# Kernel optimization log

Hardware: AMD Instinct MI355X
Metric: run time of the kernel (lower is better)

## Reference

```python
import jax, jax.numpy as jnp
import numpy as np

B, S, D_IN, D_OUT = 2, 2048, 4096, 4096


def setup_inputs() -> dict:
    key = jax.random.key(0)
    kx, kw, kb = jax.random.split(key, 3)
    x = jax.random.normal(kx, (B, S, D_IN), dtype=jnp.float32)
    weight = jax.random.normal(kw, (D_OUT, D_IN), dtype=jnp.float32)
    bias = jax.random.normal(kb, (D_OUT,), dtype=jnp.float32)
    return {"x": x, "weight": weight, "bias": bias}


def reference(x, weight, bias):
    # FdaBinary forward is simply sign(); linear with binarized weight.
    w_bin = jnp.sign(weight)  # [D_OUT, D_IN], values in {-1, 0, +1}
    # F.linear: x @ w.T + b
    out = jnp.einsum("bsd,od->bso", x, w_bin) + bias
    return out
```

## Files before the change

### kernel.cpp

```cpp
#include <hip/hip_runtime.h>
#include <hip/hip_bf16.h>
#include <stdint.h>
#include <stddef.h>

#define M_DIM 4096
#define N_DIM 4096
#define K_DIM 4096
#define BM 128
#define BN 128
#define BK 64
#define NKT (K_DIM / BK)

typedef __bf16 bf16;
typedef __attribute__((ext_vector_type(4))) __bf16 bf16x4;
typedef __attribute__((ext_vector_type(8))) __bf16 bf16x8;
typedef __attribute__((ext_vector_type(4))) float f32x4;

__global__ __launch_bounds__(256) void prep_kernel(const float* __restrict__ x,
                                                   const float* __restrict__ w,
                                                   bf16* __restrict__ xb,
                                                   bf16* __restrict__ wb) {
    const int idx = blockIdx.x * 256 + threadIdx.x;
    float4 xv = ((const float4*)x)[idx];
    bf16x4 xo;
    xo[0] = (bf16)xv.x; xo[1] = (bf16)xv.y; xo[2] = (bf16)xv.z; xo[3] = (bf16)xv.w;
    ((bf16x4*)xb)[idx] = xo;

    float4 wv = ((const float4*)w)[idx];
    bf16x4 wo;
    wo[0] = (bf16)((wv.x > 0.f) ? 1.f : ((wv.x < 0.f) ? -1.f : 0.f));
    wo[1] = (bf16)((wv.y > 0.f) ? 1.f : ((wv.y < 0.f) ? -1.f : 0.f));
    wo[2] = (bf16)((wv.z > 0.f) ? 1.f : ((wv.z < 0.f) ? -1.f : 0.f));
    wo[3] = (bf16)((wv.w > 0.f) ? 1.f : ((wv.w < 0.f) ? -1.f : 0.f));
    ((bf16x4*)wb)[idx] = wo;
}

__device__ __forceinline__ void load_lds16(const void* g, void* l) {
    __builtin_amdgcn_global_load_lds(
        (const __attribute__((address_space(1))) void*)g,
        (__attribute__((address_space(3))) void*)l, 16, 0, 0);
}

__global__ __launch_bounds__(256) void gemm_bin_kernel(const bf16* __restrict__ A,
                                                       const bf16* __restrict__ Bw,
                                                       const float* __restrict__ bias,
                                                       float* __restrict__ C) {
    __shared__ __align__(16) bf16 As[BM * BK];
    __shared__ __align__(16) bf16 Bs[BN * BK];

    const int tid  = threadIdx.x;
    const int lane = tid & 63;
    const int wave = tid >> 6;
    const int wm   = wave & 1;
    const int wn   = wave >> 1;

    const int tileM = blockIdx.y * BM;
    const int tileN = blockIdx.x * BN;

    const int rowInC = lane >> 3;
    const int q_src  = (lane & 7) ^ rowInC;

    const bf16* gA[4];
    const bf16* gB[4];
    bf16* lA[4];
    bf16* lB[4];
#pragma unroll
    for (int t = 0; t < 4; ++t) {
        const int c = wave * 4 + t;
        gA[t] = A  + (size_t)(tileM + c * 8 + rowInC) * K_DIM + q_src * 8;
        gB[t] = Bw + (size_t)(tileN + c * 8 + rowInC) * K_DIM + q_src * 8;
        lA[t] = As + c * 512;
        lB[t] = Bs + c * 512;
    }

    f32x4 acc[4][4];
#pragma unroll
    for (int i = 0; i < 4; ++i)
#pragma unroll
        for (int j = 0; j < 4; ++j)
            acc[i][j] = (f32x4){0.f, 0.f, 0.f, 0.f};

    const int l15 = lane & 15;
    const int qf  = lane >> 4;
    const int fragRowA = wm * 64 + l15;
    const int fragRowB = wn * 64 + l15;

    for (int kt = 0; kt < NKT; ++kt) {
#pragma unroll
        for (int t = 0; t < 4; ++t) {
            load_lds16(gA[t], lA[t]);
            load_lds16(gB[t], lB[t]);
            gA[t] += BK; gB[t] += BK;
        }

        __syncthreads();

#pragma unroll
        for (int kk = 0; kk < 2; ++kk) {
            const int s = (kk * 4 + qf) ^ (l15 & 7);
            bf16x8 af[4], bfr[4];
#pragma unroll
            for (int i = 0; i < 4; ++i)
                af[i] = *(const bf16x8*)&As[(fragRowA + i * 16) * BK + s * 8];
#pragma unroll
            for (int j = 0; j < 4; ++j)
                bfr[j] = *(const bf16x8*)&Bs[(fragRowB + j * 16) * BK + s * 8];

#pragma unroll
            for (int i = 0; i < 4; ++i)
#pragma unroll
                for (int j = 0; j < 4; ++j)
                    acc[i][j] = __builtin_amdgcn_mfma_f32_16x16x32_bf16(af[i], bfr[j], acc[i][j], 0, 0, 0);
        }

        __syncthreads();
    }

#pragma unroll
    for (int j = 0; j < 4; ++j) {
        const int col = tileN + wn * 64 + j * 16 + l15;
        const float bv = bias[col];
#pragma unroll
        for (int i = 0; i < 4; ++i) {
            const int row0 = tileM + wm * 64 + i * 16 + (qf << 2);
#pragma unroll
            for (int rr = 0; rr < 4; ++rr) {
                C[(size_t)(row0 + rr) * N_DIM + col] = acc[i][j][rr] + bv;
            }
        }
    }
}

extern "C" void kernel_launch(void* const* d_in, const int* in_sizes, int n_in,
                              void* d_out, int out_size, void* d_ws, size_t ws_size,
                              hipStream_t stream) {
    const float* x    = (const float*)d_in[0];
    const float* w    = (const float*)d_in[1];
    const float* bias = (const float*)d_in[2];
    float* out        = (float*)d_out;

    const int nElem = M_DIM * K_DIM;
    bf16* xb = (bf16*)d_ws;
    bf16* wb = xb + (size_t)nElem;

    prep_kernel<<<nElem / 4 / 256, 256, 0, stream>>>(x, w, xb, wb);

    dim3 grid(N_DIM / BN, M_DIM / BM);
    gemm_bin_kernel<<<grid, 256, 0, stream>>>(xb, wb, bias, out);
}
```

Before: 296.4 us.

## Enlarge GEMM tile to 256x256 with 8 waves and double-buffered LDS pipeline

Raises the block tile to 256x256 with 512 threads and double-buffers the LDS tiles. Each K-tile is split into four phases that interleave direct-to-LDS loads for the next tile with MFMA work, using explicit vmcnt waits, s_barrier and setprio. This is meant to hide global-load latency and raise arithmetic intensity per block. The cost is more registers per thread (32 accumulators), fewer blocks in the grid (256 tiles), and fragile hand-written wait counts.

```diff
diff --git a/kernel.cpp b/kernel.cpp
--- a/kernel.cpp
+++ b/kernel.cpp
@@ -6,10 +6,12 @@
 #define M_DIM 4096
 #define N_DIM 4096
 #define K_DIM 4096
-#define BM 128
-#define BN 128
+#define BM 256
+#define BN 256
 #define BK 64
 #define NKT (K_DIM / BK)
+#define BKB (BK * 2)
+#define RSTRIDE ((size_t)64 * K_DIM * 2)
 
 typedef __bf16 bf16;
 typedef __attribute__((ext_vector_type(4))) __bf16 bf16x4;
@@ -41,79 +43,108 @@
         (__attribute__((address_space(3))) void*)l, 16, 0, 0);
 }
 
-__global__ __launch_bounds__(256) void gemm_bin_kernel(const bf16* __restrict__ A,
-                                                       const bf16* __restrict__ Bw,
-                                                       const float* __restrict__ bias,
-                                                       float* __restrict__ C) {
-    __shared__ __align__(16) bf16 As[BM * BK];
-    __shared__ __align__(16) bf16 Bs[BN * BK];
+__global__ __launch_bounds__(512, 2) void gemm_bin_kernel(const bf16* __restrict__ A,
+                                                          const bf16* __restrict__ Bw,
+                                                          const float* __restrict__ bias,
+                                                          float* __restrict__ C) {
+    __shared__ __align__(16) bf16 As[2][BM * BK];
+    __shared__ __align__(16) bf16 Bs[2][BM * BK];
 
     const int tid  = threadIdx.x;
     const int lane = tid & 63;
     const int wave = tid >> 6;
-    const int wm   = wave & 1;
-    const int wn   = wave >> 1;
+    const int wm   = wave >> 2;
+    const int wn   = wave & 3;
 
     const int tileM = blockIdx.y * BM;
     const int tileN = blockIdx.x * BN;
 
     const int rowInC = lane >> 3;
     const int q_src  = (lane & 7) ^ rowInC;
+    const char* aSrc = (const char*)A  + ((size_t)(tileM + wave * 8 + rowInC) * K_DIM + q_src * 8) * 2;
+    const char* bSrc = (const char*)Bw + ((size_t)(tileN + wave * 8 + rowInC) * K_DIM + q_src * 8) * 2;
 
-    const bf16* gA[4];
-    const bf16* gB[4];
-    bf16* lA[4];
-    bf16* lB[4];
+#define STAGE_A(B_, R_, KOFF_) load_lds16(aSrc + (size_t)(R_) * RSTRIDE + (KOFF_), \
+                                          &As[B_][((R_) * 64 + wave * 8) * BK])
+#define STAGE_B(B_, R_, KOFF_) load_lds16(bSrc + (size_t)(R_) * RSTRIDE + (KOFF_), \
+                                          &Bs[B_][((R_) * 64 + wave * 8) * BK])
+
+    f32x4 acc[8][4];
 #pragma unroll
-    for (int t = 0; t < 4; ++t) {
-        const int c = wave * 4 + t;
-        gA[t] = A  + (size_t)(tileM + c * 8 + rowInC) * K_DIM + q_src * 8;
-        gB[t] = Bw + (size_t)(tileN + c * 8 + rowInC) * K_DIM + q_src * 8;
-        lA[t] = As + c * 512;
-        lB[t] = Bs + c * 512;
-    }
-
-    f32x4 acc[4][4];
-#pragma unroll
-    for (int i = 0; i < 4; ++i)
+    for (int i = 0; i < 8; ++i)
 #pragma unroll
         for (int j = 0; j < 4; ++j)
             acc[i][j] = (f32x4){0.f, 0.f, 0.f, 0.f};
 
+    bf16x8 bfr[4][2];
+
     const int l15 = lane & 15;
     const int qf  = lane >> 4;
-    const int fragRowA = wm * 64 + l15;
+    const int fragRowA = wm * 128 + l15;
     const int fragRowB = wn * 64 + l15;
+    const int s0 = (0 + qf) ^ (l15 & 7);
+    const int s1 = (4 + qf) ^ (l15 & 7);
 
-    for (int kt = 0; kt < NKT; ++kt) {
-#pragma unroll
-        for (int t = 0; t < 4; ++t) {
-            load_lds16(gA[t], lA[t]);
-            load_lds16(gB[t], lB[t]);
-            gA[t] += BK; gB[t] += BK;
+#define READ_A(B_, P_) \
+    _Pragma("unroll") \
+    for (int ii = 0; ii < 2; ++ii) { \
+        af[ii][0] = *(const bf16x8*)&As[B_][(fragRowA + (2 * (P_) + ii) * 16) * BK + s0 * 8]; \
+        af[ii][1] = *(const bf16x8*)&As[B_][(fragRowA + (2 * (P_) + ii) * 16) * BK + s1 * 8]; \
+    }
+
+#define READ_B(B_) \
+    _Pragma("unroll") \
+    for (int j = 0; j < 4; ++j) { \
+        bfr[j][0] = *(const bf16x8*)&Bs[B_][(fragRowB + j * 16) * BK + s0 * 8]; \
+        bfr[j][1] = *(const bf16x8*)&Bs[B_][(fragRowB + j * 16) * BK + s1 * 8]; \
+    }
+
+#define MFMA16(P_) \
+    _Pragma("unroll") \
+    for (int ii = 0; ii < 2; ++ii) \
+        _Pragma("unroll") \
+        for (int j = 0; j < 4; ++j) { \
+            acc[2 * (P_) + ii][j] = __builtin_amdgcn_mfma_f32_16x16x32_bf16(af[ii][0], bfr[j][0], acc[2 * (P_) + ii][j], 0, 0, 0); \
+            acc[2 * (P_) + ii][j] = __builtin_amdgcn_mfma_f32_16x16x32_bf16(af[ii][1], bfr[j][1], acc[2 * (P_) + ii][j], 0, 0, 0); \
         }
 
-        __syncthreads();
+#define PHASE(B_, P_, ISS0, ISS1, TAIL) do { \
+        bf16x8 af[2][2]; \
+        READ_A(B_, P_); \
+        if ((P_) == 0) READ_B(B_); \
+        ISS0; \
+        ISS1; \
+        __builtin_amdgcn_s_barrier(); \
+        __builtin_amdgcn_s_setprio(1); \
+        MFMA16(P_); \
+        __builtin_amdgcn_s_setprio(0); \
+        TAIL; \
+        __builtin_amdgcn_s_barrier(); \
+        __builtin_amdgcn_sched_barrier(0); \
+    } while (0)
 
-#pragma unroll
-        for (int kk = 0; kk < 2; ++kk) {
-            const int s = (kk * 4 + qf) ^ (l15 & 7);
-            bf16x8 af[4], bfr[4];
-#pragma unroll
-            for (int i = 0; i < 4; ++i)
-                af[i] = *(const bf16x8*)&As[(fragRowA + i * 16) * BK + s * 8];
-#pragma unroll
-            for (int j = 0; j < 4; ++j)
-                bfr[j] = *(const bf16x8*)&Bs[(fragRowB + j * 16) * BK + s * 8];
+#define KTILE(B_, K1_, K2_) do { \
+        PHASE(B_, 0, STAGE_A((B_) ^ 1, 1, K1_), STAGE_A((B_) ^ 1, 3, K1_), (void)0); \
+        PHASE(B_, 1, STAGE_B(B_, 0, K2_),       STAGE_B(B_, 1, K2_),       (void)0); \
+        PHASE(B_, 2, STAGE_B(B_, 2, K2_),       STAGE_B(B_, 3, K2_),       (void)0); \
+        PHASE(B_, 3, STAGE_A(B_, 0, K2_),       STAGE_A(B_, 2, K2_), \
+              asm volatile("s_waitcnt vmcnt(6)" ::: "memory")); \
+    } while (0)
 
-#pragma unroll
-            for (int i = 0; i < 4; ++i)
-#pragma unroll
-                for (int j = 0; j < 4; ++j)
-                    acc[i][j] = __builtin_amdgcn_mfma_f32_16x16x32_bf16(af[i], bfr[j], acc[i][j], 0, 0, 0);
-        }
+    STAGE_B(0, 0, 0);   STAGE_B(0, 1, 0);   STAGE_B(0, 2, 0);   STAGE_B(0, 3, 0);
+    STAGE_A(0, 0, 0);   STAGE_A(0, 2, 0);   STAGE_A(0, 1, 0);   STAGE_A(0, 3, 0);
+    STAGE_B(1, 0, BKB); STAGE_B(1, 1, BKB); STAGE_B(1, 2, BKB); STAGE_B(1, 3, BKB);
+    STAGE_A(1, 0, BKB); STAGE_A(1, 2, BKB);
+    asm volatile("s_waitcnt vmcnt(6)" ::: "memory");
+    __builtin_amdgcn_s_barrier();
+    __builtin_amdgcn_sched_barrier(0);
 
-        __syncthreads();
+    for (int kt = 0; kt < NKT; kt += 2) {
+        const int k1a = (kt + 1) * BKB;
+        const int k2a = (kt + 2 < NKT) ? (kt + 2) * BKB : 0;
+        KTILE(0, k1a, k2a);
+        const int k2b = (kt + 3 < NKT) ? (kt + 3) * BKB : 0;
+        KTILE(1, k2a, k2b);
     }
 
 #pragma unroll
@@ -121,14 +152,22 @@
         const int col = tileN + wn * 64 + j * 16 + l15;
         const float bv = bias[col];
 #pragma unroll
-        for (int i = 0; i < 4; ++i) {
-            const int row0 = tileM + wm * 64 + i * 16 + (qf << 2);
+        for (int i = 0; i < 8; ++i) {
+            const int row0 = tileM + wm * 128 + i * 16 + (qf << 2);
 #pragma unroll
             for (int rr = 0; rr < 4; ++rr) {
                 C[(size_t)(row0 + rr) * N_DIM + col] = acc[i][j][rr] + bv;
             }
         }
     }
+
+#undef STAGE_A
+#undef STAGE_B
+#undef READ_A
+#undef READ_B
+#undef MFMA16
+#undef PHASE
+#undef KTILE
 }
 
 extern "C" void kernel_launch(void* const* d_in, const int* in_sizes, int n_in,
@@ -146,5 +185,5 @@
     prep_kernel<<<nElem / 4 / 256, 256, 0, stream>>>(x, w, xb, wb);
 
     dim3 grid(N_DIM / BN, M_DIM / BM);
-    gemm_bin_kernel<<<grid, 256, 0, stream>>>(xb, wb, bias, out);
+    gemm_bin_kernel<<<grid, 512, 0, stream>>>(xb, wb, bias, out);
 }
```

After: 282.9 us. 4.6% less time.
